# Optimization experiments

Measured on AMD Instinct MI355X. Metric: run time of the kernel, lower is better.

The kernel has to match this reference:

```python
import jax, jax.numpy as jnp
import numpy as np

N = 10000
IN_DIM = 256
HID = 256
HEADS = 8
NUM_CLASSES = 40
EPS = 1e-5
NEG_SLOPE = 0.2


def gat_conv(x, src, dst, W, a_src, a_dst, bias, concat):
    # x: [N, F_in]; W: [F_in, H*C]; a_src/a_dst: [H, C]
    n = x.shape[0]
    H, C = a_src.shape
    h = (x @ W).reshape(n, H, C)                       # [N,H,C]
    s_src = jnp.einsum('nhc,hc->nh', h, a_src)         # [N,H]
    s_dst = jnp.einsum('nhc,hc->nh', h, a_dst)         # [N,H]
    score = jax.nn.leaky_relu(s_src[src] + s_dst[dst], NEG_SLOPE)  # [E,H]
    m = jax.lax.stop_gradient(jax.ops.segment_max(score, dst, num_segments=n))
    e = jnp.exp(score - m[dst])                        # [E,H]
    denom = jax.ops.segment_sum(e, dst, num_segments=n)
    alpha = e / denom[dst]                             # per-dst edge softmax
    msg = h[src] * alpha[:, :, None]                   # [E,H,C]
    out = jax.ops.segment_sum(msg, dst, num_segments=n)  # [N,H,C]
    out = out.reshape(n, H * C) if concat else out.mean(axis=1)
    return out + bias


def batch_norm(x, gamma, beta):
    mu = x.mean(axis=0)
    var = x.var(axis=0)
    return gamma * (x - mu) * jax.lax.rsqrt(var + EPS) + beta


def setup_inputs() -> dict:
    key = jax.random.key(0)
    ks = jax.random.split(key, 16)
    C0 = HID // HEADS  # 32, concat layer
    x = jax.random.normal(ks[0], (N, IN_DIM), jnp.float32)
    edge_index = jax.random.randint(ks[1], (2, 160000), 0, N, jnp.int32)
    def lin(k, fi, fo):
        return jax.random.normal(k, (fi, fo), jnp.float32) / np.sqrt(fi)
    return {
        'x': x,
        'edge_index': edge_index,
        'W0': lin(ks[2], IN_DIM, HEADS * C0),
        'a_src0': jax.random.normal(ks[3], (HEADS, C0), jnp.float32) * 0.1,
        'a_dst0': jax.random.normal(ks[4], (HEADS, C0), jnp.float32) * 0.1,
        'b0': jnp.zeros((HID,), jnp.float32),
        'g0': jnp.ones((HID,), jnp.float32),
        'be0': jnp.zeros((HID,), jnp.float32),
        'W1': lin(ks[5], HID, HEADS * HID),
        'a_src1': jax.random.normal(ks[6], (HEADS, HID), jnp.float32) * 0.1,
        'a_dst1': jax.random.normal(ks[7], (HEADS, HID), jnp.float32) * 0.1,
        'b1': jnp.zeros((HID,), jnp.float32),
        'g1': jnp.ones((HID,), jnp.float32),
        'be1': jnp.zeros((HID,), jnp.float32),
        'Wc': lin(ks[8], HID, NUM_CLASSES),
        'bc': jnp.zeros((NUM_CLASSES,), jnp.float32),
    }


def reference(x, edge_index, W0, a_src0, a_dst0, b0, g0, be0,
              W1, a_src1, a_dst1, b1, g1, be1, Wc, bc):
    n = x.shape[0]
    loops = jnp.arange(n, dtype=edge_index.dtype)
    src = jnp.concatenate([edge_index[0], loops])  # add_self_loops=True
    dst = jnp.concatenate([edge_index[1], loops])

    # layer 0: concat=True -> [N, 256]
    h = gat_conv(x, src, dst, W0, a_src0, a_dst0, b0, concat=True)
    h = jax.nn.elu(batch_norm(h, g0, be0))
    # i==0: no residual; dropout is identity at eval

    # layer 1 (last): concat=False (mean over heads) -> [N, 256]
    h_in = h
    h = gat_conv(h, src, dst, W1, a_src1, a_dst1, b1, concat=False)
    h = jax.nn.elu(batch_norm(h, g1, be1)) + h_in  # residual for i>0

    return h @ Wc + bc  # logits [N, num_classes]
```

## Files before the change

### kernel.cpp

```cpp
#include <hip/hip_runtime.h>
#include <math.h>

#define NN 10000
#define HEADS 8
#define NCLS 40
#define CHK 64
#define LOG2E 1.4426950408889634f

typedef __attribute__((ext_vector_type(8))) short short8;
typedef __attribute__((ext_vector_type(8))) unsigned short ushort8v;
typedef __attribute__((ext_vector_type(4))) float floatx4;

static __device__ __forceinline__ short f2bf(float f) {
    unsigned u = __builtin_bit_cast(unsigned, f);
    unsigned r = (u + 0x7fff + ((u >> 16) & 1)) >> 16;
    return (short)r;
}
static __device__ __forceinline__ float bf2f(unsigned short u) {
    unsigned x = ((unsigned)u) << 16;
    return __builtin_bit_cast(float, x);
}
static __device__ __forceinline__ void gl2lds16(const void* g, void* l) {
    __builtin_amdgcn_global_load_lds(
        (const __attribute__((address_space(1))) unsigned int*)g,
        (__attribute__((address_space(3))) unsigned int*)l, 16, 0, 0);
}

__global__ __launch_bounds__(256) void gemm_bf16_w128(
    const float* __restrict__ Af32, const short* __restrict__ Bt,
    short* __restrict__ Cbf,
    const float* __restrict__ asrc, const float* __restrict__ adst,
    float* __restrict__ s0,
    const int* __restrict__ esrc, const int* __restrict__ edst,
    int* __restrict__ cursor, int* __restrict__ elist, int E, int scatBlocks,
    const float* __restrict__ W1, const float* __restrict__ a_src1,
    const float* __restrict__ a_dst1, float* __restrict__ v1,
    short* __restrict__ W1pT,
    int gemmBlocks, int gridY,
    int M, int Nn, int K, float alpha)
{
    __shared__ short As[64 * 64];
    __shared__ short Bs[128 * 64];
    const int tid = threadIdx.x;
    if ((int)blockIdx.x >= gemmBlocks) {
        int td = (int)blockIdx.x - gemmBlocks;
        if (td < scatBlocks) {
            int e = td * 256 + tid;
            if (e < E) {
                int dn = edst[e];
                int pos = atomicAdd(&cursor[dn], 1);
                elist[pos] = esrc[e];
            }
            return;
        }
        td -= scatBlocks;
        if (td < 16) {
            int idx = td * 256 + tid;
            int f = idx >> 4, j = idx & 15;
            int h = j & 7;
            const float* a = (j < 8) ? a_src1 : a_dst1;
            float s = 0.f;
            for (int c = 0; c < 256; c++)
                s += W1[f * 2048 + h * 256 + c] * a[h * 256 + c];
            v1[idx] = s;
            return;
        }
        td -= 16;
        {
            float (*tile)[33] = (float(*)[33])As;
            int h = td >> 6, f0 = ((td >> 3) & 7) * 32, c0 = (td & 7) * 32;
            int tx = tid & 31, ty = tid >> 5;
            for (int r = ty; r < 32; r += 8)
                tile[r][tx] = W1[(size_t)(f0 + r) * 2048 + h * 256 + c0 + tx];
            __syncthreads();
            for (int r = ty; r < 32; r += 8)
                W1pT[(size_t)(c0 + r) * 2048 + h * 256 + f0 + tx] = f2bf(tile[tx][r]);
            return;
        }
    }
    const int w = tid >> 6, L = tid & 63;
    const int quad = L >> 4, lr = L & 15;
    const int d = blockIdx.x;
    const int by = (d >> 4) * 8 + (d & 7);
    const int bx = (d >> 3) & 1;
    if (by >= gridY) return;
    const int col0 = bx * 128, row0 = by * 64;

    const int schunk = (L & 7) ^ (L >> 3);
    const int sarow = w * 16 + (L >> 3);
    int ga0 = row0 + sarow;     if (ga0 > M - 1) ga0 = M - 1;
    int ga1 = row0 + sarow + 8; if (ga1 > M - 1) ga1 = M - 1;
    const float* axp0 = Af32 + (size_t)ga0 * K + schunk * 8;
    const float* axp1 = Af32 + (size_t)ga1 * K + schunk * 8;
    short* alw0 = &As[w * 1024 + L * 8];
    short* alw1 = &As[w * 1024 + 512 + L * 8];
    const int sbrow = w * 32 + (L >> 3);
    int gb[4];
    #pragma unroll
    for (int c = 0; c < 4; c++) {
        gb[c] = col0 + sbrow + c * 8;
        if (gb[c] > Nn - 1) gb[c] = Nn - 1;
    }
    const short* bgp0 = Bt + (size_t)gb[0] * K + schunk * 8;
    const short* bgp1 = Bt + (size_t)gb[1] * K + schunk * 8;
    const short* bgp2 = Bt + (size_t)gb[2] * K + schunk * 8;
    const short* bgp3 = Bt + (size_t)gb[3] * K + schunk * 8;
    short* blp0 = &Bs[w * 2048];
    short* blp1 = &Bs[w * 2048 + 512];
    short* blp2 = &Bs[w * 2048 + 1024];
    short* blp3 = &Bs[w * 2048 + 1536];

    floatx4 acc[4][2];
    const floatx4 zf = {0.f, 0.f, 0.f, 0.f};
    #pragma unroll
    for (int i = 0; i < 4; i++)
        #pragma unroll
        for (int j = 0; j < 2; j++) acc[i][j] = zf;

    for (int k0 = 0; k0 < K; k0 += 64) {
        gl2lds16(bgp0 + k0, blp0);
        gl2lds16(bgp1 + k0, blp1);
        gl2lds16(bgp2 + k0, blp2);
        gl2lds16(bgp3 + k0, blp3);
        {
            floatx4 va0 = *(const floatx4*)(axp0 + k0);
            floatx4 va1 = *(const floatx4*)(axp0 + k0 + 4);
            floatx4 vb0 = *(const floatx4*)(axp1 + k0);
            floatx4 vb1 = *(const floatx4*)(axp1 + k0 + 4);
            short8 o0, o1;
            #pragma unroll
            for (int q = 0; q < 8; q++) {
                o0[q] = f2bf(q < 4 ? va0[q & 3] : va1[q & 3]);
                o1[q] = f2bf(q < 4 ? vb0[q & 3] : vb1[q & 3]);
            }
            *(short8*)alw0 = o0;
            *(short8*)alw1 = o1;
        }
        __syncthreads();
        #pragma unroll
        for (int ks = 0; ks < 2; ks++) {
            const int sl = ((ks * 4 + quad) ^ (lr & 7)) * 8;
            short8 bfr[2];
            #pragma unroll
            for (int j = 0; j < 2; j++)
                bfr[j] = *(const short8*)&Bs[(w * 32 + j * 16 + lr) * 64 + sl];
            #pragma unroll
            for (int i = 0; i < 4; i++) {
                short8 afr = *(const short8*)&As[(i * 16 + lr) * 64 + sl];
                #pragma unroll
                for (int j = 0; j < 2; j++)
                    acc[i][j] = __builtin_amdgcn_mfma_f32_16x16x32_bf16(afr, bfr[j], acc[i][j], 0, 0, 0);
            }
        }
        __syncthreads();
    }
    #pragma unroll
    for (int j = 0; j < 2; j++) {
        int ccol = col0 + w * 32 + j * 16 + lr;
        if (ccol >= Nn) continue;
        #pragma unroll
        for (int i = 0; i < 4; i++) {
            #pragma unroll
            for (int r = 0; r < 4; r++) {
                int crow = row0 + i * 16 + quad * 4 + r;
                if (crow < M)
                    Cbf[(size_t)crow * Nn + ccol] = f2bf(alpha * acc[i][j][r]);
            }
        }
    }
    {
        const int head = bx * 4 + w;
        float as0 = asrc[col0 + w * 32 + lr];
        float as1 = asrc[col0 + w * 32 + 16 + lr];
        float ad0 = adst[col0 + w * 32 + lr];
        float ad1 = adst[col0 + w * 32 + 16 + lr];
        #pragma unroll
        for (int i = 0; i < 4; i++) {
            #pragma unroll
            for (int r = 0; r < 4; r++) {
                float ps = acc[i][0][r] * as0 + acc[i][1][r] * as1;
                float pd = acc[i][0][r] * ad0 + acc[i][1][r] * ad1;
                #pragma unroll
                for (int off = 1; off < 16; off <<= 1) {
                    ps += __shfl_xor(ps, off, 64);
                    pd += __shfl_xor(pd, off, 64);
                }
                if (lr == 0) {
                    int crow = row0 + i * 16 + quad * 4 + r;
                    if (crow < M) {
                        s0[crow * 16 + head] = alpha * ps;
                        s0[crow * 16 + 8 + head] = alpha * pd;
                    }
                }
            }
        }
    }
}

__global__ __launch_bounds__(256) void gemm1_db(
    const short* __restrict__ A, const short* __restrict__ Bt,
    float* __restrict__ C, float* __restrict__ stats,
    int gridY, int M, int Nn, int K, float alpha)
{
    __shared__ short As[2][32 * 64];
    __shared__ short Bs[2][128 * 64];
    const int tid = threadIdx.x;
    const int w = tid >> 6, L = tid & 63;
    const int quad = L >> 4, lr = L & 15;
    const int d = blockIdx.x;
    const int by = (d >> 4) * 8 + (d & 7);
    const int bx = (d >> 3) & 1;
    if (by >= gridY) return;
    const int col0 = bx * 128, row0 = by * 32;

    const int schunk = (L & 7) ^ (L >> 3);
    int ga = row0 + w * 8 + (L >> 3); if (ga > M - 1) ga = M - 1;
    const short* agp = A + (size_t)ga * K + schunk * 8;
    const int sbrow = w * 32 + (L >> 3);
    int gb[4];
    #pragma unroll
    for (int c = 0; c < 4; c++) {
        gb[c] = col0 + sbrow + c * 8;
        if (gb[c] > Nn - 1) gb[c] = Nn - 1;
    }
    const short* bgp0 = Bt + (size_t)gb[0] * K + schunk * 8;
    const short* bgp1 = Bt + (size_t)gb[1] * K + schunk * 8;
    const short* bgp2 = Bt + (size_t)gb[2] * K + schunk * 8;
    const short* bgp3 = Bt + (size_t)gb[3] * K + schunk * 8;

    floatx4 acc[2][2];
    const floatx4 zf = {0.f, 0.f, 0.f, 0.f};
    #pragma unroll
    for (int i = 0; i < 2; i++)
        #pragma unroll
        for (int j = 0; j < 2; j++) acc[i][j] = zf;

    const int nt = K >> 6;
    gl2lds16(agp,  &As[0][w * 512]);
    gl2lds16(bgp0, &Bs[0][w * 2048]);
    gl2lds16(bgp1, &Bs[0][w * 2048 + 512]);
    gl2lds16(bgp2, &Bs[0][w * 2048 + 1024]);
    gl2lds16(bgp3, &Bs[0][w * 2048 + 1536]);
    __syncthreads();
    int cur = 0;
    for (int t = 0; t < nt; t++) {
        if (t + 1 < nt) {
            const int k0 = (t + 1) << 6;
            const int nb = cur ^ 1;
            gl2lds16(agp + k0,  &As[nb][w * 512]);
            gl2lds16(bgp0 + k0, &Bs[nb][w * 2048]);
            gl2lds16(bgp1 + k0, &Bs[nb][w * 2048 + 512]);
            gl2lds16(bgp2 + k0, &Bs[nb][w * 2048 + 1024]);
            gl2lds16(bgp3 + k0, &Bs[nb][w * 2048 + 1536]);
        }
        #pragma unroll
        for (int ks = 0; ks < 2; ks++) {
            const int sl = ((ks * 4 + quad) ^ (lr & 7)) * 8;
            short8 bfr[2];
            #pragma unroll
            for (int j = 0; j < 2; j++)
                bfr[j] = *(const short8*)&Bs[cur][(w * 32 + j * 16 + lr) * 64 + sl];
            #pragma unroll
            for (int i = 0; i < 2; i++) {
                short8 afr = *(const short8*)&As[cur][(i * 16 + lr) * 64 + sl];
                #pragma unroll
                for (int j = 0; j < 2; j++)
                    acc[i][j] = __builtin_amdgcn_mfma_f32_16x16x32_bf16(afr, bfr[j], acc[i][j], 0, 0, 0);
            }
        }
        __syncthreads();
        cur ^= 1;
    }
    float s[2] = {0.f, 0.f}, s2[2] = {0.f, 0.f};
    #pragma unroll
    for (int j = 0; j < 2; j++) {
        int ccol = col0 + w * 32 + j * 16 + lr;
        if (ccol >= Nn) continue;
        #pragma unroll
        for (int i = 0; i < 2; i++) {
            #pragma unroll
            for (int r = 0; r < 4; r++) {
                int crow = row0 + i * 16 + quad * 4 + r;
                if (crow < M) {
                    float v = alpha * acc[i][j][r];
                    C[(size_t)crow * Nn + ccol] = v;
                    s[j] += v; s2[j] += v * v;
                }
            }
        }
    }
    #pragma unroll
    for (int j = 0; j < 2; j++) {
        s[j]  += __shfl_xor(s[j], 16, 64);  s[j]  += __shfl_xor(s[j], 32, 64);
        s2[j] += __shfl_xor(s2[j], 16, 64); s2[j] += __shfl_xor(s2[j], 32, 64);
    }
    if (L < 16) {
        #pragma unroll
        for (int j = 0; j < 2; j++) {
            int ccol = col0 + w * 32 + j * 16 + L;
            if (ccol < Nn) {
                atomicAdd(&stats[ccol], s[j]);
                atomicAdd(&stats[256 + ccol], s2[j]);
            }
        }
    }
}

__global__ __launch_bounds__(256) void classifier_fused(
    const float* __restrict__ X, const float* __restrict__ stats,
    const float* __restrict__ g, const float* __restrict__ be,
    const unsigned short* __restrict__ resid,
    const short* __restrict__ Bt, float* __restrict__ C,
    const float* __restrict__ bias, int M, int Nn, int K)
{
    __shared__ short As[2][32 * 64];
    __shared__ short Bs[2][64 * 64];
    const int tid = threadIdx.x;
    const int w = tid >> 6, L = tid & 63;
    const int quad = L >> 4, lr = L & 15;
    const int row0 = blockIdx.x * 32;

    const int schunk = (L & 7) ^ (L >> 3);
    int ga = row0 + w * 8 + (L >> 3); if (ga > M - 1) ga = M - 1;
    int gbrow = w * 16 + (L >> 3);
    int gb0 = gbrow;     if (gb0 > Nn - 1) gb0 = Nn - 1;
    int gb1 = gbrow + 8; if (gb1 > Nn - 1) gb1 = Nn - 1;
    const float* xg = X + (size_t)ga * K + schunk * 8;
    const unsigned short* rg = resid + (size_t)ga * K + schunk * 8;
    const short* bgp0 = Bt + (size_t)gb0 * K + schunk * 8;
    const short* bgp1 = Bt + (size_t)gb1 * K + schunk * 8;

    floatx4 acc[2];
    const floatx4 zf = {0.f, 0.f, 0.f, 0.f};
    acc[0] = zf; acc[1] = zf;
    const float invN = 1.0f / NN;
    const int nt = K >> 6;

    floatx4 xa, xb2; ushort8v rv;
    xa  = *(const floatx4*)(xg);
    xb2 = *(const floatx4*)(xg + 4);
    rv  = *(const ushort8v*)(rg);
    gl2lds16(bgp0, &Bs[0][w * 1024]);
    gl2lds16(bgp1, &Bs[0][w * 1024 + 512]);
    {
        const int c = schunk * 8;
        short8 av;
        #pragma unroll
        for (int q = 0; q < 8; q++) {
            float m  = stats[c + q] * invN;
            float sq = stats[256 + c + q] * invN;
            float rs = rsqrtf(sq - m * m + 1e-5f) * g[c + q];
            float sh = be[c + q] - m * rs;
            float v = (q < 4 ? xa[q & 3] : xb2[q & 3]) * rs + sh;
            v = (v > 0.f) ? v : (expf(v) - 1.f);
            v += bf2f(rv[q]);
            av[q] = f2bf(v);
        }
        *(short8*)&As[0][w * 512 + L * 8] = av;
    }
    __syncthreads();
    int cur = 0;
    for (int t = 0; t < nt; t++) {
        floatx4 nxa, nxb2; ushort8v nrv;
        if (t + 1 < nt) {
            const int k0 = (t + 1) << 6;
            nxa  = *(const floatx4*)(xg + k0);
            nxb2 = *(const floatx4*)(xg + k0 + 4);
            nrv  = *(const ushort8v*)(rg + k0);
            gl2lds16(bgp0 + k0, &Bs[cur ^ 1][w * 1024]);
            gl2lds16(bgp1 + k0, &Bs[cur ^ 1][w * 1024 + 512]);
        }
        #pragma unroll
        for (int ks = 0; ks < 2; ks++) {
            const int sl = ((ks * 4 + quad) ^ (lr & 7)) * 8;
            short8 bfr = *(const short8*)&Bs[cur][(w * 16 + lr) * 64 + sl];
            #pragma unroll
            for (int i = 0; i < 2; i++) {
                short8 afr = *(const short8*)&As[cur][(i * 16 + lr) * 64 + sl];
                acc[i] = __builtin_amdgcn_mfma_f32_16x16x32_bf16(afr, bfr, acc[i], 0, 0, 0);
            }
        }
        if (t + 1 < nt) {
            const int c = schunk * 8 + ((t + 1) << 6);
            short8 av;
            #pragma unroll
            for (int q = 0; q < 8; q++) {
                float m  = stats[c + q] * invN;
                float sq = stats[256 + c + q] * invN;
                float rs = rsqrtf(sq - m * m + 1e-5f) * g[c + q];
                float sh = be[c + q] - m * rs;
                float v = (q < 4 ? nxa[q & 3] : nxb2[q & 3]) * rs + sh;
                v = (v > 0.f) ? v : (expf(v) - 1.f);
                v += bf2f(nrv[q]);
                av[q] = f2bf(v);
            }
            *(short8*)&As[cur ^ 1][w * 512 + L * 8] = av;
        }
        __syncthreads();
        cur ^= 1;
    }
    const int ccol = w * 16 + lr;
    if (ccol < Nn) {
        float bv = bias ? bias[ccol] : 0.f;
        #pragma unroll
        for (int i = 0; i < 2; i++) {
            #pragma unroll
            for (int r = 0; r < 4; r++) {
                int crow = row0 + i * 16 + quad * 4 + r;
                if (crow < M) C[(size_t)crow * Nn + ccol] = acc[i][r] + bv;
            }
        }
    }
}

__global__ __launch_bounds__(256) void prep_a(
    const float* __restrict__ W0, const float* __restrict__ Wc,
    const int* __restrict__ edst, int E,
    short* __restrict__ W0T, short* __restrict__ WcT,
    int* __restrict__ counts)
{
    const int b = blockIdx.x, t = threadIdx.x;
    if (b < 256) {
        W0T[b * 256 + t] = f2bf(W0[t * 256 + b]);
    } else if (b < 296) {
        int o = b - 256;
        WcT[o * 256 + t] = f2bf(Wc[t * 40 + o]);
    } else {
        int e = (b - 296) * 256 + t;
        if (e < E) atomicAdd(&counts[edst[e]], 1);
    }
}

__global__ __launch_bounds__(1024) void scan_kernel(
    int* __restrict__ counts, int* __restrict__ offsets,
    int* __restrict__ cursor, int* __restrict__ elist)
{
    __shared__ int wsum[16];
    const int t = threadIdx.x, lane = t & 63, wid = t >> 6;
    constexpr int P = 10;
    const int base = t * P;
    int deg[P], loc[P];
    int s = 0;
    #pragma unroll
    for (int j = 0; j < P; j++) {
        int i = base + j;
        loc[j] = s;
        deg[j] = (i < NN) ? counts[i] + 1 : 0;
        s += deg[j];
    }
    int inc = s;
    #pragma unroll
    for (int off = 1; off < 64; off <<= 1) {
        int tv = __shfl_up(inc, off, 64);
        if (lane >= off) inc += tv;
    }
    if (lane == 63) wsum[wid] = inc;
    __syncthreads();
    if (t < 16) {
        int v = wsum[t];
        int winc = v;
        #pragma unroll
        for (int off = 1; off < 16; off <<= 1) {
            int tv = __shfl_up(winc, off, 16);
            if (t >= off) winc += tv;
        }
        wsum[t] = winc - v;
    }
    __syncthreads();
    int excl = inc - s + wsum[wid];
    #pragma unroll
    for (int j = 0; j < P; j++) {
        int i = base + j;
        if (i < NN) {
            int o = excl + loc[j];
            counts[i] = deg[j];
            offsets[i] = o;
            elist[o] = i;
            cursor[i] = o + 1;
        }
    }
}

__global__ __launch_bounds__(256) void agg0_fused(
    const unsigned short* __restrict__ h0b, const float* __restrict__ s0,
    const int* __restrict__ offsets, const int* __restrict__ counts,
    const int* __restrict__ elist, float* __restrict__ out)
{
    __shared__ float pw_s[4][CHK * 8];
    __shared__ int   sn_s[4][CHK];
    const int wid = threadIdx.x >> 6, L = threadIdx.x & 63;
    const int n = blockIdx.x * 4 + wid;
    float* pw = pw_s[wid];
    int*   sw = sn_s[wid];
    const int deg = counts[n], start = offsets[n];
    const int hL = L >> 3;

    floatx4 sda = *(const floatx4*)(s0 + n * 16 + 8);
    floatx4 sdb = *(const floatx4*)(s0 + n * 16 + 12);
    float sd[8] = {sda[0], sda[1], sda[2], sda[3], sdb[0], sdb[1], sdb[2], sdb[3]};
    float lp[8] = {0.f, 0.f, 0.f, 0.f, 0.f, 0.f, 0.f, 0.f};
    float a0 = 0.f, a1 = 0.f, a2 = 0.f, a3 = 0.f;

    for (int e0 = 0; e0 < deg; e0 += CHK) {
        int ch = deg - e0; if (ch > CHK) ch = CHK;
        if (L < ch) {
            int sn = elist[start + e0 + L];
            sw[L] = sn;
            floatx4 ssa = *(const floatx4*)(s0 + sn * 16);
            floatx4 ssb = *(const floatx4*)(s0 + sn * 16 + 4);
            float ss[8] = {ssa[0], ssa[1], ssa[2], ssa[3], ssb[0], ssb[1], ssb[2], ssb[3]};
            float p[8];
            #pragma unroll
            for (int h = 0; h < 8; h++) {
                float v = ss[h] + sd[h];
                v = (v > 0.f) ? v : 0.2f * v;
                p[h] = exp2f(v * LOG2E);
                lp[h] += p[h];
            }
            floatx4 p0 = {p[0], p[1], p[2], p[3]};
            floatx4 p1 = {p[4], p[5], p[6], p[7]};
            *(floatx4*)&pw[L * 8] = p0;
            *(floatx4*)&pw[L * 8 + 4] = p1;
        }
        int e = 0;
        for (; e + 4 <= ch; e += 4) {
            float wA = pw[e * 8 + hL];
            float wB = pw[e * 8 + 8 + hL];
            float wC = pw[e * 8 + 16 + hL];
            float wD = pw[e * 8 + 24 + hL];
            ushort4 vA = *(const ushort4*)(h0b + (size_t)sw[e] * 256 + 4 * L);
            ushort4 vB = *(const ushort4*)(h0b + (size_t)sw[e + 1] * 256 + 4 * L);
            ushort4 vC = *(const ushort4*)(h0b + (size_t)sw[e + 2] * 256 + 4 * L);
            ushort4 vD = *(const ushort4*)(h0b + (size_t)sw[e + 3] * 256 + 4 * L);
            a0 += wA * bf2f(vA.x); a1 += wA * bf2f(vA.y);
            a2 += wA * bf2f(vA.z); a3 += wA * bf2f(vA.w);
            a0 += wB * bf2f(vB.x); a1 += wB * bf2f(vB.y);
            a2 += wB * bf2f(vB.z); a3 += wB * bf2f(vB.w);
            a0 += wC * bf2f(vC.x); a1 += wC * bf2f(vC.y);
            a2 += wC * bf2f(vC.z); a3 += wC * bf2f(vC.w);
            a0 += wD * bf2f(vD.x); a1 += wD * bf2f(vD.y);
            a2 += wD * bf2f(vD.z); a3 += wD * bf2f(vD.w);
        }
        for (; e + 2 <= ch; e += 2) {
            float wA = pw[e * 8 + hL];
            float wB = pw[e * 8 + 8 + hL];
            ushort4 vA = *(const ushort4*)(h0b + (size_t)sw[e] * 256 + 4 * L);
            ushort4 vB = *(const ushort4*)(h0b + (size_t)sw[e + 1] * 256 + 4 * L);
            a0 += wA * bf2f(vA.x); a1 += wA * bf2f(vA.y);
            a2 += wA * bf2f(vA.z); a3 += wA * bf2f(vA.w);
            a0 += wB * bf2f(vB.x); a1 += wB * bf2f(vB.y);
            a2 += wB * bf2f(vB.z); a3 += wB * bf2f(vB.w);
        }
        if (e < ch) {
            float wA = pw[e * 8 + hL];
            ushort4 vA = *(const ushort4*)(h0b + (size_t)sw[e] * 256 + 4 * L);
            a0 += wA * bf2f(vA.x); a1 += wA * bf2f(vA.y);
            a2 += wA * bf2f(vA.z); a3 += wA * bf2f(vA.w);
        }
    }
    #pragma unroll
    for (int off = 1; off < 64; off <<= 1)
        #pragma unroll
        for (int h = 0; h < 8; h++)
            lp[h] += __shfl_xor(lp[h], off, 64);
    float inv = 1.f / lp[hL];
    floatx4 o = {a0 * inv, a1 * inv, a2 * inv, a3 * inv};
    *(floatx4*)(out + (size_t)n * 256 + 4 * L) = o;
}

__global__ __launch_bounds__(256) void agg1_full(
    const unsigned short* __restrict__ hb, const float* __restrict__ s1,
    const int* __restrict__ offsets, const int* __restrict__ counts,
    const int* __restrict__ elist, short* __restrict__ aggout)
{
    __shared__ float pw_s[4][CHK * 8];
    __shared__ int   sn_s[4][CHK];
    const int wid = threadIdx.x >> 6, L = threadIdx.x & 63;
    const int n = blockIdx.x * 4 + wid;
    float* pw = pw_s[wid];
    int*   sw = sn_s[wid];
    const int deg = counts[n], start = offsets[n];

    floatx4 sda = *(const floatx4*)(s1 + n * 16 + 8);
    floatx4 sdb = *(const floatx4*)(s1 + n * 16 + 12);
    float sd[8] = {sda[0], sda[1], sda[2], sda[3], sdb[0], sdb[1], sdb[2], sdb[3]};
    float lp[8] = {0.f, 0.f, 0.f, 0.f, 0.f, 0.f, 0.f, 0.f};
    float acc[8][4];
    #pragma unroll
    for (int h = 0; h < 8; h++)
        #pragma unroll
        for (int f = 0; f < 4; f++) acc[h][f] = 0.f;

    for (int e0 = 0; e0 < deg; e0 += CHK) {
        int ch = deg - e0; if (ch > CHK) ch = CHK;
        if (L < ch) {
            int sn = elist[start + e0 + L];
            sw[L] = sn;
            floatx4 ssa = *(const floatx4*)(s1 + sn * 16);
            floatx4 ssb = *(const floatx4*)(s1 + sn * 16 + 4);
            float ss[8] = {ssa[0], ssa[1], ssa[2], ssa[3], ssb[0], ssb[1], ssb[2], ssb[3]};
            float p[8];
            #pragma unroll
            for (int h = 0; h < 8; h++) {
                float v = ss[h] + sd[h];
                v = (v > 0.f) ? v : 0.2f * v;
                p[h] = exp2f(v * LOG2E);
                lp[h] += p[h];
            }
            floatx4 p0 = {p[0], p[1], p[2], p[3]};
            floatx4 p1 = {p[4], p[5], p[6], p[7]};
            *(floatx4*)&pw[L * 8] = p0;
            *(floatx4*)&pw[L * 8 + 4] = p1;
        }
        int e = 0;
        for (; e + 4 <= ch; e += 4) {
            ushort4 vA = *(const ushort4*)(hb + (size_t)sw[e] * 256 + 4 * L);
            ushort4 vB = *(const ushort4*)(hb + (size_t)sw[e + 1] * 256 + 4 * L);
            ushort4 vC = *(const ushort4*)(hb + (size_t)sw[e + 2] * 256 + 4 * L);
            ushort4 vD = *(const ushort4*)(hb + (size_t)sw[e + 3] * 256 + 4 * L);
            floatx4 p0A = *(const floatx4*)&pw[e * 8];
            floatx4 p1A = *(const floatx4*)&pw[e * 8 + 4];
            floatx4 p0B = *(const floatx4*)&pw[e * 8 + 8];
            floatx4 p1B = *(const floatx4*)&pw[e * 8 + 12];
            floatx4 p0C = *(const floatx4*)&pw[e * 8 + 16];
            floatx4 p1C = *(const floatx4*)&pw[e * 8 + 20];
            floatx4 p0D = *(const floatx4*)&pw[e * 8 + 24];
            floatx4 p1D = *(const floatx4*)&pw[e * 8 + 28];
            float a0 = bf2f(vA.x), a1 = bf2f(vA.y), a2 = bf2f(vA.z), a3 = bf2f(vA.w);
            #pragma unroll
            for (int h = 0; h < 4; h++) {
                acc[h][0] += p0A[h] * a0;     acc[h][1] += p0A[h] * a1;
                acc[h][2] += p0A[h] * a2;     acc[h][3] += p0A[h] * a3;
                acc[h + 4][0] += p1A[h] * a0; acc[h + 4][1] += p1A[h] * a1;
                acc[h + 4][2] += p1A[h] * a2; acc[h + 4][3] += p1A[h] * a3;
            }
            float b0 = bf2f(vB.x), b1 = bf2f(vB.y), b2 = bf2f(vB.z), b3 = bf2f(vB.w);
            #pragma unroll
            for (int h = 0; h < 4; h++) {
                acc[h][0] += p0B[h] * b0;     acc[h][1] += p0B[h] * b1;
                acc[h][2] += p0B[h] * b2;     acc[h][3] += p0B[h] * b3;
                acc[h + 4][0] += p1B[h] * b0; acc[h + 4][1] += p1B[h] * b1;
                acc[h + 4][2] += p1B[h] * b2; acc[h + 4][3] += p1B[h] * b3;
            }
            float c0 = bf2f(vC.x), c1 = bf2f(vC.y), c2 = bf2f(vC.z), c3 = bf2f(vC.w);
            #pragma unroll
            for (int h = 0; h < 4; h++) {
                acc[h][0] += p0C[h] * c0;     acc[h][1] += p0C[h] * c1;
                acc[h][2] += p0C[h] * c2;     acc[h][3] += p0C[h] * c3;
                acc[h + 4][0] += p1C[h] * c0; acc[h + 4][1] += p1C[h] * c1;
                acc[h + 4][2] += p1C[h] * c2; acc[h + 4][3] += p1C[h] * c3;
            }
            float d0 = bf2f(vD.x), d1 = bf2f(vD.y), d2 = bf2f(vD.z), d3 = bf2f(vD.w);
            #pragma unroll
            for (int h = 0; h < 4; h++) {
                acc[h][0] += p0D[h] * d0;     acc[h][1] += p0D[h] * d1;
                acc[h][2] += p0D[h] * d2;     acc[h][3] += p0D[h] * d3;
                acc[h + 4][0] += p1D[h] * d0; acc[h + 4][1] += p1D[h] * d1;
                acc[h + 4][2] += p1D[h] * d2; acc[h + 4][3] += p1D[h] * d3;
            }
        }
        for (; e + 2 <= ch; e += 2) {
            floatx4 p0A = *(const floatx4*)&pw[e * 8];
            floatx4 p1A = *(const floatx4*)&pw[e * 8 + 4];
            floatx4 p0B = *(const floatx4*)&pw[e * 8 + 8];
            floatx4 p1B = *(const floatx4*)&pw[e * 8 + 12];
            ushort4 vA = *(const ushort4*)(hb + (size_t)sw[e] * 256 + 4 * L);
            ushort4 vB = *(const ushort4*)(hb + (size_t)sw[e + 1] * 256 + 4 * L);
            float a0 = bf2f(vA.x), a1 = bf2f(vA.y), a2 = bf2f(vA.z), a3 = bf2f(vA.w);
            float b0 = bf2f(vB.x), b1 = bf2f(vB.y), b2 = bf2f(vB.z), b3 = bf2f(vB.w);
            #pragma unroll
            for (int h = 0; h < 4; h++) {
                acc[h][0] += p0A[h] * a0;     acc[h][1] += p0A[h] * a1;
                acc[h][2] += p0A[h] * a2;     acc[h][3] += p0A[h] * a3;
                acc[h + 4][0] += p1A[h] * a0; acc[h + 4][1] += p1A[h] * a1;
                acc[h + 4][2] += p1A[h] * a2; acc[h + 4][3] += p1A[h] * a3;
            }
            #pragma unroll
            for (int h = 0; h < 4; h++) {
                acc[h][0] += p0B[h] * b0;     acc[h][1] += p0B[h] * b1;
                acc[h][2] += p0B[h] * b2;     acc[h][3] += p0B[h] * b3;
                acc[h + 4][0] += p1B[h] * b0; acc[h + 4][1] += p1B[h] * b1;
                acc[h + 4][2] += p1B[h] * b2; acc[h + 4][3] += p1B[h] * b3;
            }
        }
        if (e < ch) {
            floatx4 p0A = *(const floatx4*)&pw[e * 8];
            floatx4 p1A = *(const floatx4*)&pw[e * 8 + 4];
            ushort4 vA = *(const ushort4*)(hb + (size_t)sw[e] * 256 + 4 * L);
            float a0 = bf2f(vA.x), a1 = bf2f(vA.y), a2 = bf2f(vA.z), a3 = bf2f(vA.w);
            #pragma unroll
            for (int h = 0; h < 4; h++) {
                acc[h][0] += p0A[h] * a0;     acc[h][1] += p0A[h] * a1;
                acc[h][2] += p0A[h] * a2;     acc[h][3] += p0A[h] * a3;
                acc[h + 4][0] += p1A[h] * a0; acc[h + 4][1] += p1A[h] * a1;
                acc[h + 4][2] += p1A[h] * a2; acc[h + 4][3] += p1A[h] * a3;
            }
        }
    }
    #pragma unroll
    for (int off = 1; off < 64; off <<= 1)
        #pragma unroll
        for (int h = 0; h < 8; h++)
            lp[h] += __shfl_xor(lp[h], off, 64);
    #pragma unroll
    for (int h = 0; h < 8; h++) {
        float inv = 1.f / lp[h];
        short4 o = {f2bf(acc[h][0] * inv), f2bf(acc[h][1] * inv),
                    f2bf(acc[h][2] * inv), f2bf(acc[h][3] * inv)};
        *(short4*)(aggout + (size_t)n * 2048 + h * 256 + 4 * L) = o;
    }
}

__global__ __launch_bounds__(1024) void bn_stats_kernel(
    const float* __restrict__ x, float* __restrict__ stats, int n)
{
    __shared__ float red[16][512];
    const int t = threadIdx.x;
    const int sub = t >> 6, c4 = (t & 63) * 4;
    floatx4 s = {0.f, 0.f, 0.f, 0.f}, s2 = {0.f, 0.f, 0.f, 0.f};
    for (int r = blockIdx.x * 16 + sub; r < n; r += gridDim.x * 16) {
        floatx4 v = *(const floatx4*)(x + (size_t)r * 256 + c4);
        s += v; s2 += v * v;
    }
    #pragma unroll
    for (int k = 0; k < 4; k++) {
        red[sub][c4 + k] = s[k];
        red[sub][256 + c4 + k] = s2[k];
    }
    __syncthreads();
    if (t < 512) {
        float acc = 0.f;
        #pragma unroll
        for (int i = 0; i < 16; i++) acc += red[i][t];
        atomicAdd(&stats[t], acc);
    }
}

__global__ __launch_bounds__(256) void bnapply_score1(
    const float* __restrict__ xg, const float* __restrict__ stats,
    const float* __restrict__ g, const float* __restrict__ be,
    const float* __restrict__ v1, short* __restrict__ hactb, float* __restrict__ s1)
{
    __shared__ float row[256];
    __shared__ float part[16][17];
    const int n = blockIdx.x, t = threadIdx.x;
    const float invN = 1.0f / NN;
    float mu = stats[t] * invN;
    float var = stats[256 + t] * invN - mu * mu;
    float v = g[t] * (xg[(size_t)n * 256 + t] - mu) * rsqrtf(var + 1e-5f) + be[t];
    v = (v > 0.f) ? v : (expf(v) - 1.f);
    hactb[(size_t)n * 256 + t] = f2bf(v);
    row[t] = v;
    __syncthreads();
    int j = t & 15, f0 = t >> 4;
    float p = 0.f;
    #pragma unroll
    for (int k = 0; k < 16; k++)
        p += row[f0 * 16 + k] * v1[(f0 * 16 + k) * 16 + j];
    part[f0][j] = p;
    __syncthreads();
    if (t < 16) {
        float s = 0.f;
        #pragma unroll
        for (int k = 0; k < 16; k++) s += part[k][t];
        s1[n * 16 + t] = s;
    }
}

extern "C" void kernel_launch(void* const* d_in, const int* in_sizes, int n_in,
                              void* d_out, int out_size, void* d_ws, size_t ws_size,
                              hipStream_t stream) {
    const float* x      = (const float*)d_in[0];
    const int*   eidx   = (const int*)d_in[1];
    const float* W0     = (const float*)d_in[2];
    const float* a_src0 = (const float*)d_in[3];
    const float* a_dst0 = (const float*)d_in[4];
    const float* g0     = (const float*)d_in[6];
    const float* be0    = (const float*)d_in[7];
    const float* W1     = (const float*)d_in[8];
    const float* a_src1 = (const float*)d_in[9];
    const float* a_dst1 = (const float*)d_in[10];
    const float* g1     = (const float*)d_in[12];
    const float* be1    = (const float*)d_in[13];
    const float* Wc     = (const float*)d_in[14];
    const float* bc     = (const float*)d_in[15];
    float* out = (float*)d_out;

    const int E = in_sizes[1] / 2;
    const int* esrc = eidx;
    const int* edst = eidx + E;

    char* ws = (char*)d_ws;
    size_t off = 0;
    auto alloc = [&](size_t bytes) {
        void* p = ws + off;
        off += (bytes + 255) & ~(size_t)255;
        return p;
    };
    float* stats   = (float*)alloc(1024 * 4);
    int*   counts  = (int*)alloc(NN * 4);
    float* out1    = (float*)alloc((size_t)NN * 256 * 4);
    short* h0b     = (short*)alloc((size_t)NN * 256 * 2);
    float* s0      = (float*)alloc((size_t)NN * 16 * 4);
    float* s1      = (float*)alloc((size_t)NN * 16 * 4);
    float* v1      = (float*)alloc(4096 * 4);
    float* h_gat0  = (float*)alloc((size_t)NN * 256 * 4);
    short* hactb   = (short*)alloc((size_t)NN * 256 * 2);
    short* agg1bf  = (short*)alloc((size_t)NN * 2048 * 2);
    short* W0T     = (short*)alloc((size_t)256 * 256 * 2);
    short* W1pT    = (short*)alloc((size_t)256 * 2048 * 2);
    short* WcT     = (short*)alloc((size_t)64 * 256 * 2);
    int* offsets   = (int*)alloc((NN + 16) * 4);
    int* cursor    = (int*)alloc(NN * 4);
    int* elist     = (int*)alloc((size_t)(E + NN) * 4);

    float* stats0 = stats;
    float* stats1 = stats + 512;

    hipMemsetAsync(stats, 0, 1024 * 4 + NN * 4, stream);

    const int cntBlocks = (E + 255) / 256;

    prep_a<<<296 + cntBlocks, 256, 0, stream>>>(W0, Wc, edst, E, W0T, WcT, counts);

    scan_kernel<<<1, 1024, 0, stream>>>(counts, offsets, cursor, elist);

    const int gy = (NN + 63) / 64;
    const int gB = 16 * ((gy + 7) / 8);

    gemm_bf16_w128<<<gB + cntBlocks + 528, 256, 0, stream>>>(
        x, W0T, h0b,
        a_src0, a_dst0, s0,
        esrc, edst, cursor, elist, E, cntBlocks,
        W1, a_src1, a_dst1, v1, W1pT,
        gB, gy, NN, 256, 256, 1.0f);

    agg0_fused<<<NN / 4, 256, 0, stream>>>(
        (const unsigned short*)h0b, s0, offsets, counts, elist, h_gat0);
    bn_stats_kernel<<<64, 1024, 0, stream>>>(h_gat0, stats0, NN);
    bnapply_score1<<<NN, 256, 0, stream>>>(h_gat0, stats0, g0, be0, v1, hactb, s1);

    agg1_full<<<NN / 4, 256, 0, stream>>>(
        (const unsigned short*)hactb, s1, offsets, counts, elist, agg1bf);
    const int gy1 = (NN + 31) / 32;
    const int gB1 = 16 * ((gy1 + 7) / 8);
    gemm1_db<<<gB1, 256, 0, stream>>>(
        agg1bf, W1pT, out1, stats1, gy1, NN, 256, 2048, 0.125f);

    classifier_fused<<<(NN + 31) / 32, 256, 0, stream>>>(
        out1, stats1, g1, be1, (const unsigned short*)hactb,
        WcT, out, bc, NN, NCLS, 256);
}
```

Before: 245.4 us.

## Fuse BatchNorm statistics into layer-0 aggregation with last-block reduction

Result: slower. 427.6 us (+74.3%).

```diff
diff --git a/kernel.cpp b/kernel.cpp
--- a/kernel.cpp
+++ b/kernel.cpp
@@ -484,10 +484,13 @@
 __global__ __launch_bounds__(256) void agg0_fused(
     const unsigned short* __restrict__ h0b, const float* __restrict__ s0,
     const int* __restrict__ offsets, const int* __restrict__ counts,
-    const int* __restrict__ elist, float* __restrict__ out)
+    const int* __restrict__ elist, float* __restrict__ out,
+    float* __restrict__ pstats, unsigned int* __restrict__ donec,
+    float* __restrict__ stats0)
 {
     __shared__ float pw_s[4][CHK * 8];
     __shared__ int   sn_s[4][CHK];
+    __shared__ int   lastBlk;
     const int wid = threadIdx.x >> 6, L = threadIdx.x & 63;
     const int n = blockIdx.x * 4 + wid;
     float* pw = pw_s[wid];
@@ -566,6 +569,37 @@
     float inv = 1.f / lp[hL];
     floatx4 o = {a0 * inv, a1 * inv, a2 * inv, a3 * inv};
     *(floatx4*)(out + (size_t)n * 256 + 4 * L) = o;
+
+    #pragma unroll
+    for (int k = 0; k < 4; k++) {
+        pw[4 * L + k] = o[k];
+        pw[256 + 4 * L + k] = o[k] * o[k];
+    }
+    __syncthreads();
+    {
+        const int t = threadIdx.x;
+        float ps  = pw_s[0][t] + pw_s[1][t] + pw_s[2][t] + pw_s[3][t];
+        float ps2 = pw_s[0][256 + t] + pw_s[1][256 + t] + pw_s[2][256 + t] + pw_s[3][256 + t];
+        const int slot = (int)(blockIdx.x & 63);
+        atomicAdd(&pstats[slot * 512 + t], ps);
+        atomicAdd(&pstats[slot * 512 + 256 + t], ps2);
+        __threadfence();
+        __syncthreads();
+        if (t == 0)
+            lastBlk = (atomicAdd(donec, 1u) == (unsigned)(gridDim.x - 1));
+        __syncthreads();
+        if (lastBlk) {
+            __threadfence();
+            float s = 0.f, s2v = 0.f;
+            #pragma unroll
+            for (int k = 0; k < 64; k++) {
+                s   += pstats[k * 512 + t];
+                s2v += pstats[k * 512 + 256 + t];
+            }
+            stats0[t] = s;
+            stats0[256 + t] = s2v;
+        }
+    }
 }
 
 __global__ __launch_bounds__(256) void agg1_full(
@@ -708,31 +742,6 @@
         short4 o = {f2bf(acc[h][0] * inv), f2bf(acc[h][1] * inv),
                     f2bf(acc[h][2] * inv), f2bf(acc[h][3] * inv)};
         *(short4*)(aggout + (size_t)n * 2048 + h * 256 + 4 * L) = o;
-    }
-}
-
-__global__ __launch_bounds__(1024) void bn_stats_kernel(
-    const float* __restrict__ x, float* __restrict__ stats, int n)
-{
-    __shared__ float red[16][512];
-    const int t = threadIdx.x;
-    const int sub = t >> 6, c4 = (t & 63) * 4;
-    floatx4 s = {0.f, 0.f, 0.f, 0.f}, s2 = {0.f, 0.f, 0.f, 0.f};
-    for (int r = blockIdx.x * 16 + sub; r < n; r += gridDim.x * 16) {
-        floatx4 v = *(const floatx4*)(x + (size_t)r * 256 + c4);
-        s += v; s2 += v * v;
-    }
-    #pragma unroll
-    for (int k = 0; k < 4; k++) {
-        red[sub][c4 + k] = s[k];
-        red[sub][256 + c4 + k] = s2[k];
-    }
-    __syncthreads();
-    if (t < 512) {
-        float acc = 0.f;
-        #pragma unroll
-        for (int i = 0; i < 16; i++) acc += red[i][t];
-        atomicAdd(&stats[t], acc);
     }
 }
 
@@ -798,6 +807,8 @@
         return p;
     };
     float* stats   = (float*)alloc(1024 * 4);
+    float* pstats  = (float*)alloc(64 * 512 * 4);
+    unsigned int* donec = (unsigned int*)alloc(256);
     int*   counts  = (int*)alloc(NN * 4);
     float* out1    = (float*)alloc((size_t)NN * 256 * 4);
     short* h0b     = (short*)alloc((size_t)NN * 256 * 2);
@@ -817,7 +828,7 @@
     float* stats0 = stats;
     float* stats1 = stats + 512;
 
-    hipMemsetAsync(stats, 0, 1024 * 4 + NN * 4, stream);
+    hipMemsetAsync(stats, 0, 1024 * 4 + 64 * 512 * 4 + 256 + NN * 4, stream);
 
     const int cntBlocks = (E + 255) / 256;
 
@@ -836,8 +847,8 @@
         gB, gy, NN, 256, 256, 1.0f);
 
     agg0_fused<<<NN / 4, 256, 0, stream>>>(
-        (const unsigned short*)h0b, s0, offsets, counts, elist, h_gat0);
-    bn_stats_kernel<<<64, 1024, 0, stream>>>(h_gat0, stats0, NN);
+        (const unsigned short*)h0b, s0, offsets, counts, elist, h_gat0,
+        pstats, donec, stats0);
     bnapply_score1<<<NN, 256, 0, stream>>>(h_gat0, stats0, g0, be0, v1, hactb, s1);
 
     agg1_full<<<NN / 4, 256, 0, stream>>>(
```
